# Kernel tuning notes

Measured on AMD Instinct MI355X. Metric: run time of the kernel, lower is better.

## Reference

```python
import jax, jax.numpy as jnp
import numpy as np

L, D, H, BS = 12, 768, 12, 512
VU, VD, NM, B = 512, 512, 438, 8
HD = D // H
EPS = 1e-5


def _ln(x, w, b):
    m = jnp.mean(x, axis=-1, keepdims=True)
    v = jnp.mean(jnp.square(x - m), axis=-1, keepdims=True)
    return (x - m) * jax.lax.rsqrt(v + EPS) * w + b


def setup_inputs() -> dict:
    key = jax.random.key(0)
    ks = jax.random.split(key, 16)
    s = 0.02
    inp = {
        'idx_up': jax.random.randint(ks[0], (B, BS), 0, VU),
        'idx_down': jax.random.randint(ks[1], (B, BS), 0, VD),
        'cond': jax.random.normal(ks[2], (B, BS, NM), dtype=jnp.float32),
        'tok_emb_up': s * jax.random.normal(ks[3], (VU, D), dtype=jnp.float32),
        'tok_emb_down': s * jax.random.normal(ks[4], (VD, D), dtype=jnp.float32),
        'pos_emb': s * jax.random.normal(ks[5], (1, 3 * BS, D), dtype=jnp.float32),
        'cond_w': s * jax.random.normal(ks[6], (NM, D), dtype=jnp.float32),
        'cond_b': jnp.zeros((D,), jnp.float32),
        'ln1_w': jnp.ones((L, D), jnp.float32),
        'ln1_b': jnp.zeros((L, D), jnp.float32),
        'ln2_w': jnp.ones((L, D), jnp.float32),
        'ln2_b': jnp.zeros((L, D), jnp.float32),
        'Wq': s * jax.random.normal(ks[7], (L, D, D), dtype=jnp.float32),
        'bq': jnp.zeros((L, D), jnp.float32),
        'Wk': s * jax.random.normal(ks[8], (L, D, D), dtype=jnp.float32),
        'bk': jnp.zeros((L, D), jnp.float32),
        'Wv': s * jax.random.normal(ks[9], (L, D, D), dtype=jnp.float32),
        'bv': jnp.zeros((L, D), jnp.float32),
        'Wp': s * jax.random.normal(ks[10], (L, D, D), dtype=jnp.float32),
        'bp': jnp.zeros((L, D), jnp.float32),
        'W1': s * jax.random.normal(ks[11], (L, D, 4 * D), dtype=jnp.float32),
        'b1': jnp.zeros((L, 4 * D), jnp.float32),
        'W2': s * jax.random.normal(ks[12], (L, 4 * D, D), dtype=jnp.float32),
        'b2': jnp.zeros((L, D), jnp.float32),
    }
    return inp


def reference(idx_up, idx_down, cond, tok_emb_up, tok_emb_down, pos_emb,
              cond_w, cond_b, ln1_w, ln1_b, ln2_w, ln2_b,
              Wq, bq, Wk, bk, Wv, bv, Wp, bp, W1, b1, W2, b2):
    b, t = idx_up.shape
    T = 3 * t
    # embeddings: [cond_emb | up | down] along seq
    x = jnp.concatenate([
        cond @ cond_w + cond_b,
        tok_emb_up[idx_up],
        tok_emb_down[idx_down],
    ], axis=1)
    pos = jnp.concatenate([
        pos_emb[:, :t, :],
        pos_emb[:, BS:BS + t, :],
        pos_emb[:, 2 * BS:2 * BS + t, :],
    ], axis=1)
    x = x + pos

    # 3x3-tiled causal mask over the three t-length segments
    tri = jnp.tril(jnp.ones((t, t), dtype=bool))
    mask = jnp.tile(tri, (3, 3))  # [T, T]
    scale = 1.0 / np.sqrt(HD)

    for l in range(L):
        h = _ln(x, ln1_w[l], ln1_b[l])
        q = (h @ Wq[l] + bq[l]).reshape(b, T, H, HD)
        k = (h @ Wk[l] + bk[l]).reshape(b, T, H, HD)
        v = (h @ Wv[l] + bv[l]).reshape(b, T, H, HD)
        att = jnp.einsum('bihd,bjhd->bhij', q, k) * scale
        att = jnp.where(mask, att, -jnp.inf)
        att = jax.nn.softmax(att, axis=-1)
        y = jnp.einsum('bhij,bjhd->bihd', att, v).reshape(b, T, D)
        x = x + (y @ Wp[l] + bp[l])

        h = _ln(x, ln2_w[l], ln2_b[l])
        h = jax.nn.gelu(h @ W1[l] + b1[l], approximate=False)
        x = x + (h @ W2[l] + b2[l])
    return x
```

## Files before the change

### kernel.cpp

```cpp
#include <hip/hip_runtime.h>
#include <cstdint>
#include <cstddef>

typedef uint16_t u16;
typedef __attribute__((ext_vector_type(8))) __bf16 bf16x8;
typedef __attribute__((ext_vector_type(4))) float f32x4;

#define DEVI static __device__ __forceinline__

DEVI u16 f2bf(float f) {
    union { float f; uint32_t u; } x; x.f = f;
    uint32_t r = (x.u + 0x7fffu + ((x.u >> 16) & 1u)) >> 16;
    return (u16)r;
}

DEVI void async_load16(const u16* g, const u16* l) {
    __builtin_amdgcn_global_load_lds(
        (__attribute__((address_space(1))) uint32_t*)(uintptr_t)g,
        (__attribute__((address_space(3))) uint32_t*)(uintptr_t)l,
        16, 0, 0);
}

enum { EP_QKV = 0, EP_RESID = 1, EP_GELU = 2, EP_COND = 3 };

template<int EP>
__global__ __launch_bounds__(256)
void gemm_k(const u16* __restrict__ A, const u16* __restrict__ Bt,
            int M, int N, int K,
            const float* __restrict__ bias0, const float* __restrict__ bias1,
            const float* __restrict__ bias2,
            float* __restrict__ xout, u16* __restrict__ bfout,
            const float* __restrict__ pos)
{
    __shared__ u16 As[128 * 32];
    __shared__ u16 Bs[128 * 32];
    const int tid = threadIdx.x;
    const int m0 = blockIdx.y * 128;
    const int n0 = blockIdx.x * 128;
    const int lane = tid & 63;
    const int wave = tid >> 6;
    const int quad = lane >> 4;
    const int l16 = lane & 15;
    const int wr = (wave >> 1) * 64;
    const int wc = (wave & 1) * 64;

    f32x4 acc[4][4] = {};

    const int srow = tid >> 2;
    const int sseg = tid & 3;
    const u16* aptr = A + (size_t)(m0 + srow) * K + sseg * 8;
    const u16* bptr = Bt + (size_t)(n0 + srow) * K + sseg * 8;

    for (int kb = 0; kb < K; kb += 32) {
        __syncthreads();
        async_load16(aptr + kb, As + tid * 8);
        async_load16(aptr + (size_t)64 * K + kb, As + 2048 + tid * 8);
        async_load16(bptr + kb, Bs + tid * 8);
        async_load16(bptr + (size_t)64 * K + kb, Bs + 2048 + tid * 8);
        __syncthreads();
        bf16x8 af[4], bfr[4];
        #pragma unroll
        for (int i = 0; i < 4; i++)
            af[i] = *(const bf16x8*)(As + (wr + i * 16 + l16) * 32 + quad * 8);
        #pragma unroll
        for (int i = 0; i < 4; i++)
            bfr[i] = *(const bf16x8*)(Bs + (wc + i * 16 + l16) * 32 + quad * 8);
        #pragma unroll
        for (int mi = 0; mi < 4; mi++)
            #pragma unroll
            for (int ni = 0; ni < 4; ni++)
                acc[mi][ni] = __builtin_amdgcn_mfma_f32_16x16x32_bf16(
                    af[mi], bfr[ni], acc[mi][ni], 0, 0, 0);
    }

    #pragma unroll
    for (int mi = 0; mi < 4; mi++) {
        const int rbase = m0 + wr + mi * 16 + quad * 4;
        #pragma unroll
        for (int ni = 0; ni < 4; ni++) {
            const int col = n0 + wc + ni * 16 + l16;
            float bias;
            if (EP == EP_QKV)
                bias = (col < 768) ? bias0[col]
                     : (col < 1536) ? bias1[col - 768] : bias2[col - 1536];
            else
                bias = bias0[col];
            #pragma unroll
            for (int r = 0; r < 4; r++) {
                const int row = rbase + r;
                float v = acc[mi][ni][r] + bias;
                if (EP == EP_QKV) {
                    bfout[(size_t)row * N + col] = f2bf(v);
                } else if (EP == EP_GELU) {
                    v = 0.5f * v * (1.0f + erff(v * 0.70710678f));
                    bfout[(size_t)row * N + col] = f2bf(v);
                } else if (EP == EP_RESID) {
                    xout[(size_t)row * N + col] += v;
                } else {
                    const int b = row >> 9, i = row & 511;
                    xout[((size_t)(b * 1536 + i)) * 768 + col] =
                        v + pos[(size_t)i * 768 + col];
                }
            }
        }
    }
}

__global__ __launch_bounds__(256)
void ln_k(const float* __restrict__ x, const float* __restrict__ w,
          const float* __restrict__ b, u16* __restrict__ h)
{
    const int row = blockIdx.x * 4 + (threadIdx.x >> 6);
    const int lane = threadIdx.x & 63;
    const float* xr = x + (size_t)row * 768;
    float vals[12];
    float s = 0.f;
    #pragma unroll
    for (int i = 0; i < 12; i++) { vals[i] = xr[lane + i * 64]; s += vals[i]; }
    #pragma unroll
    for (int o = 32; o; o >>= 1) s += __shfl_xor(s, o);
    const float mean = s * (1.f / 768.f);
    float vs = 0.f;
    #pragma unroll
    for (int i = 0; i < 12; i++) { float d = vals[i] - mean; vs += d * d; }
    #pragma unroll
    for (int o = 32; o; o >>= 1) vs += __shfl_xor(vs, o);
    const float rstd = rsqrtf(vs * (1.f / 768.f) + 1e-5f);
    u16* hr = h + (size_t)row * 768;
    #pragma unroll
    for (int i = 0; i < 12; i++) {
        const int c = lane + i * 64;
        hr[c] = f2bf((vals[i] - mean) * rstd * w[c] + b[c]);
    }
}

__global__ __launch_bounds__(256)
void attn_k(const u16* __restrict__ qkv, u16* __restrict__ y)
{
    __shared__ u16 Ks[64 * 64];
    __shared__ u16 Vt[64 * 64];
    __shared__ u16 Ps[4][16 * 72];
    const int qt = blockIdx.x, hh = blockIdx.y, b = blockIdx.z;
    const int tid = threadIdx.x, wave = tid >> 6, lane = tid & 63;
    const int quad = lane >> 4, l16 = lane & 15;
    const int l7 = l16 & 7;
    const size_t RS = 2304;
    const u16* qb  = qkv + (size_t)b * 1536 * RS + hh * 64;
    const u16* kbp = qb + 768;
    const u16* vbp = qb + 1536;

    bf16x8 qf[2];
    {
        const u16* qr = qb + (size_t)(qt * 64 + wave * 16 + l16) * RS + quad * 8;
        qf[0] = *(const bf16x8*)(qr);
        qf[1] = *(const bf16x8*)(qr + 32);
    }

    f32x4 o_acc[4] = {};
    float m_i = -1e30f, l_i = 0.f;
    const float scale = 0.125f;

    const int srow = tid >> 2;
    const int sseg = tid & 3;
    const int vkey = tid & 63, vw = tid >> 6;
    const int kmax = qt & 7;

    for (int seg3 = 0; seg3 < 3; seg3++) {
        for (int k8 = 0; k8 <= kmax; k8++) {
            const int kt = seg3 * 8 + k8;
            const bool diag = (k8 == kmax);
            __syncthreads();
            {
                const u16* krow = kbp + (size_t)(kt * 64 + srow) * RS;
                bf16x8 c0 = *(const bf16x8*)(krow + sseg * 8);
                bf16x8 c1 = *(const bf16x8*)(krow + (sseg + 4) * 8);
                const int sw = srow & 7;
                *(bf16x8*)(Ks + srow * 64 + ((sseg    ) ^ sw) * 8) = c0;
                *(bf16x8*)(Ks + srow * 64 + ((sseg + 4) ^ sw) * 8) = c1;
            }
            {
                const u16* vrow = vbp + (size_t)(kt * 64 + vkey) * RS;
                const int kc = vkey >> 3, ko = vkey & 7;
                #pragma unroll
                for (int i = 0; i < 2; i++) {
                    bf16x8 vv = *(const bf16x8*)(vrow + (vw + i * 4) * 8);
                    const u16* vr = (const u16*)&vv;
                    #pragma unroll
                    for (int j = 0; j < 8; j++) {
                        const int hd = (vw + i * 4) * 8 + j;
                        Vt[hd * 64 + ((kc ^ j) * 8) + ko] = vr[j];
                    }
                }
            }
            __syncthreads();

            f32x4 sacc[4] = {};
            #pragma unroll
            for (int st = 0; st < 2; st++)
                #pragma unroll
                for (int kb = 0; kb < 4; kb++) {
                    bf16x8 kf = *(const bf16x8*)(Ks + (kb * 16 + l16) * 64 +
                                    ((st * 4 + quad) ^ l7) * 8);
                    sacc[kb] = __builtin_amdgcn_mfma_f32_16x16x32_bf16(
                        kf, qf[st], sacc[kb], 0, 0, 0);
                }

            float sv[16];
            const int thr = wave * 16 + l16;
            #pragma unroll
            for (int kb = 0; kb < 4; kb++)
                #pragma unroll
                for (int r = 0; r < 4; r++) {
                    float v = sacc[kb][r] * scale;
                    if (diag && (kb * 16 + quad * 4 + r > thr)) v = -1e30f;
                    sv[kb * 4 + r] = v;
                }
            float mx = sv[0];
            #pragma unroll
            for (int i = 1; i < 16; i++) mx = fmaxf(mx, sv[i]);
            mx = fmaxf(mx, __shfl_xor(mx, 16));
            mx = fmaxf(mx, __shfl_xor(mx, 32));
            const float mnew = fmaxf(m_i, mx);
            const float alpha = __expf(m_i - mnew);
            float ps = 0.f;
            #pragma unroll
            for (int i = 0; i < 16; i++) { sv[i] = __expf(sv[i] - mnew); ps += sv[i]; }
            ps += __shfl_xor(ps, 16);
            ps += __shfl_xor(ps, 32);
            l_i = l_i * alpha + ps;
            m_i = mnew;
            #pragma unroll
            for (int n = 0; n < 4; n++) {
                o_acc[n][0] *= alpha; o_acc[n][1] *= alpha;
                o_acc[n][2] *= alpha; o_acc[n][3] *= alpha;
            }
            #pragma unroll
            for (int kb = 0; kb < 4; kb++) {
                ushort4 p4;
                p4.x = f2bf(sv[kb * 4 + 0]); p4.y = f2bf(sv[kb * 4 + 1]);
                p4.z = f2bf(sv[kb * 4 + 2]); p4.w = f2bf(sv[kb * 4 + 3]);
                *(ushort4*)(&Ps[wave][l16 * 72 + kb * 16 + quad * 4]) = p4;
            }
            #pragma unroll
            for (int st = 0; st < 2; st++) {
                bf16x8 pf = *(const bf16x8*)(&Ps[wave][l16 * 72 + st * 32 + quad * 8]);
                #pragma unroll
                for (int n = 0; n < 4; n++) {
                    bf16x8 vf = *(const bf16x8*)(Vt + (n * 16 + l16) * 64 +
                                    ((st * 4 + quad) ^ l7) * 8);
                    o_acc[n] = __builtin_amdgcn_mfma_f32_16x16x32_bf16(
                        vf, pf, o_acc[n], 0, 0, 0);
                }
            }
        }
    }

    const float inv = 1.f / l_i;
    u16* yr = y + ((size_t)b * 1536 + qt * 64 + wave * 16 + l16) * 768 + hh * 64;
    #pragma unroll
    for (int n = 0; n < 4; n++) {
        ushort4 o4;
        o4.x = f2bf(o_acc[n][0] * inv);
        o4.y = f2bf(o_acc[n][1] * inv);
        o4.z = f2bf(o_acc[n][2] * inv);
        o4.w = f2bf(o_acc[n][3] * inv);
        *(ushort4*)(yr + n * 16 + quad * 4) = o4;
    }
}

__global__ __launch_bounds__(256)
void cvt_layer_k(const float* __restrict__ Wq, const float* __restrict__ Wk,
                 const float* __restrict__ Wv, const float* __restrict__ Wp,
                 const float* __restrict__ W1, const float* __restrict__ W2,
                 u16* __restrict__ Wt)
{
    int id = blockIdx.x;
    const float* src; u16* dst; int Kd, Nd;
    if (id < 2304) {
        const int m = id / 576; id -= m * 576;
        src = (m == 0) ? Wq : (m == 1) ? Wk : (m == 2) ? Wv : Wp;
        dst = Wt + (size_t)m * 589824; Kd = 768; Nd = 768;
    } else if (id < 4608) {
        id -= 2304; src = W1; dst = Wt + (size_t)4 * 589824; Kd = 768; Nd = 3072;
    } else {
        id -= 4608; src = W2; dst = Wt + (size_t)4 * 589824 + 2359296; Kd = 3072; Nd = 768;
    }
    const int tn_n = Nd >> 5;
    const int tk = id / tn_n, tn = id - tk * tn_n;
    __shared__ float tile[32][33];
    const int tx = threadIdx.x & 31, ty = threadIdx.x >> 5;
    #pragma unroll
    for (int i = 0; i < 4; i++)
        tile[ty + i * 8][tx] = src[(size_t)(tk * 32 + ty + i * 8) * Nd + tn * 32 + tx];
    __syncthreads();
    #pragma unroll
    for (int i = 0; i < 4; i++)
        dst[(size_t)(tn * 32 + ty + i * 8) * Kd + tk * 32 + tx] = f2bf(tile[tx][ty + i * 8]);
}

__global__ void cvt_cond_k(const float* __restrict__ cond, u16* __restrict__ condb) {
    const int r = blockIdx.x, k = threadIdx.x;
    condb[(size_t)r * 448 + k] = (k < 438) ? f2bf(cond[(size_t)r * 438 + k]) : (u16)0;
}
__global__ void cvt_condw_k(const float* __restrict__ cw, u16* __restrict__ cwt) {
    const int n = blockIdx.x, k = threadIdx.x;
    cwt[(size_t)n * 448 + k] = (k < 438) ? f2bf(cw[(size_t)k * 768 + n]) : (u16)0;
}

__global__ void embed_k(const int* __restrict__ iu, const int* __restrict__ idn,
                        const float* __restrict__ eu, const float* __restrict__ ed,
                        const float* __restrict__ pos, float* __restrict__ x)
{
    const int t = blockIdx.x * 256 + threadIdx.x;
    const int d4 = t % 192;
    const int row = t / 192;
    const int b = row >> 10, pl = row & 1023;
    const float* src; int posrow;
    if (pl < 512) { src = eu + (size_t)iu[b * 512 + pl] * 768; posrow = 512 + pl; }
    else { src = ed + (size_t)idn[b * 512 + pl - 512] * 768; posrow = 1024 + (pl - 512); }
    float4 v = ((const float4*)src)[d4];
    const float4 p = ((const float4*)(pos + (size_t)posrow * 768))[d4];
    v.x += p.x; v.y += p.y; v.z += p.z; v.w += p.w;
    ((float4*)(x + ((size_t)b * 1536 + posrow) * 768))[d4] = v;
}

extern "C" void kernel_launch(void* const* d_in, const int* in_sizes, int n_in,
                              void* d_out, int out_size, void* d_ws, size_t ws_size,
                              hipStream_t stream)
{
    const int*   idx_up   = (const int*)d_in[0];
    const int*   idx_down = (const int*)d_in[1];
    const float* cond     = (const float*)d_in[2];
    const float* emb_up   = (const float*)d_in[3];
    const float* emb_down = (const float*)d_in[4];
    const float* pos      = (const float*)d_in[5];
    const float* cond_w   = (const float*)d_in[6];
    const float* cond_b   = (const float*)d_in[7];
    const float* ln1_w    = (const float*)d_in[8];
    const float* ln1_b    = (const float*)d_in[9];
    const float* ln2_w    = (const float*)d_in[10];
    const float* ln2_b    = (const float*)d_in[11];
    const float* Wq = (const float*)d_in[12]; const float* bq = (const float*)d_in[13];
    const float* Wk = (const float*)d_in[14]; const float* bk = (const float*)d_in[15];
    const float* Wv = (const float*)d_in[16]; const float* bv = (const float*)d_in[17];
    const float* Wp = (const float*)d_in[18]; const float* bp = (const float*)d_in[19];
    const float* W1 = (const float*)d_in[20]; const float* b1 = (const float*)d_in[21];
    const float* W2 = (const float*)d_in[22]; const float* b2 = (const float*)d_in[23];

    float* x = (float*)d_out;

    u16* h     = (u16*)d_ws;
    u16* qkv   = h + 9437184;
    u16* y     = qkv + 28311552;
    u16* h1    = y + 9437184;
    u16* Wt    = h1 + 37748736;
    u16* condb = Wt + 7077888;
    u16* cwt   = condb + 1835008;

    cvt_cond_k<<<4096, 448, 0, stream>>>(cond, condb);
    cvt_condw_k<<<768, 448, 0, stream>>>(cond_w, cwt);
    embed_k<<<6144, 256, 0, stream>>>(idx_up, idx_down, emb_up, emb_down, pos, x);
    gemm_k<EP_COND><<<dim3(6, 32), 256, 0, stream>>>(condb, cwt, 4096, 768, 448,
        cond_b, nullptr, nullptr, x, nullptr, pos);

    for (int l = 0; l < 12; l++) {
        cvt_layer_k<<<6912, 256, 0, stream>>>(
            Wq + (size_t)l * 589824, Wk + (size_t)l * 589824, Wv + (size_t)l * 589824,
            Wp + (size_t)l * 589824, W1 + (size_t)l * 2359296, W2 + (size_t)l * 2359296, Wt);
        ln_k<<<3072, 256, 0, stream>>>(x, ln1_w + l * 768, ln1_b + l * 768, h);
        gemm_k<EP_QKV><<<dim3(18, 96), 256, 0, stream>>>(h, Wt, 12288, 2304, 768,
            bq + l * 768, bk + l * 768, bv + l * 768, nullptr, qkv, nullptr);
        attn_k<<<dim3(24, 12, 8), 256, 0, stream>>>(qkv, y);
        gemm_k<EP_RESID><<<dim3(6, 96), 256, 0, stream>>>(y, Wt + (size_t)3 * 589824,
            12288, 768, 768, bp + l * 768, nullptr, nullptr, x, nullptr, nullptr);
        ln_k<<<3072, 256, 0, stream>>>(x, ln2_w + l * 768, ln2_b + l * 768, h);
        gemm_k<EP_GELU><<<dim3(24, 96), 256, 0, stream>>>(h, Wt + (size_t)4 * 589824,
            12288, 3072, 768, b1 + l * 3072, nullptr, nullptr, nullptr, h1, nullptr);
        gemm_k<EP_RESID><<<dim3(6, 96), 256, 0, stream>>>(h1,
            Wt + (size_t)4 * 589824 + 2359296, 12288, 768, 3072,
            b2 + l * 768, nullptr, nullptr, x, nullptr, nullptr);
    }
}
```

Measured before the change: 6.463 ms.

## Pair causal query tiles per block and read K fragments directly from global

Each attention block now handles two query tiles, a and 7-a, within a segment, so the causal work per block is equal and the grid is halved. The K tile is no longer staged in LDS; MFMA operands are loaded straight from global memory. The softmax scale and log2(e) are folded into Q so the kernel can use exp2f, and launch bounds request 4 blocks per CU. The trade-off is that each wave now reads K from global/L2 redundantly, and Q picks up an extra bf16 rounding after scaling.

```diff
diff --git a/kernel.cpp b/kernel.cpp
--- a/kernel.cpp
+++ b/kernel.cpp
@@ -134,137 +134,138 @@
     }
 }
 
-__global__ __launch_bounds__(256)
+__global__ __launch_bounds__(256, 4)
 void attn_k(const u16* __restrict__ qkv, u16* __restrict__ y)
 {
-    __shared__ u16 Ks[64 * 64];
     __shared__ u16 Vt[64 * 64];
     __shared__ u16 Ps[4][16 * 72];
-    const int qt = blockIdx.x, hh = blockIdx.y, b = blockIdx.z;
+    const int seg = blockIdx.x >> 2, a = blockIdx.x & 3;
+    const int hh = blockIdx.y, b = blockIdx.z;
     const int tid = threadIdx.x, wave = tid >> 6, lane = tid & 63;
-    const int quad = lane >> 4, l16 = lane & 15;
-    const int l7 = l16 & 7;
+    const int quad = lane >> 4, l16 = lane & 15, l7 = l16 & 7;
     const size_t RS = 2304;
     const u16* qb  = qkv + (size_t)b * 1536 * RS + hh * 64;
     const u16* kbp = qb + 768;
     const u16* vbp = qb + 1536;
-
-    bf16x8 qf[2];
-    {
-        const u16* qr = qb + (size_t)(qt * 64 + wave * 16 + l16) * RS + quad * 8;
-        qf[0] = *(const bf16x8*)(qr);
-        qf[1] = *(const bf16x8*)(qr + 32);
-    }
-
-    f32x4 o_acc[4] = {};
-    float m_i = -1e30f, l_i = 0.f;
-    const float scale = 0.125f;
-
-    const int srow = tid >> 2;
-    const int sseg = tid & 3;
     const int vkey = tid & 63, vw = tid >> 6;
-    const int kmax = qt & 7;
-
-    for (int seg3 = 0; seg3 < 3; seg3++) {
-        for (int k8 = 0; k8 <= kmax; k8++) {
-            const int kt = seg3 * 8 + k8;
-            const bool diag = (k8 == kmax);
-            __syncthreads();
-            {
-                const u16* krow = kbp + (size_t)(kt * 64 + srow) * RS;
-                bf16x8 c0 = *(const bf16x8*)(krow + sseg * 8);
-                bf16x8 c1 = *(const bf16x8*)(krow + (sseg + 4) * 8);
-                const int sw = srow & 7;
-                *(bf16x8*)(Ks + srow * 64 + ((sseg    ) ^ sw) * 8) = c0;
-                *(bf16x8*)(Ks + srow * 64 + ((sseg + 4) ^ sw) * 8) = c1;
-            }
-            {
-                const u16* vrow = vbp + (size_t)(kt * 64 + vkey) * RS;
-                const int kc = vkey >> 3, ko = vkey & 7;
-                #pragma unroll
-                for (int i = 0; i < 2; i++) {
-                    bf16x8 vv = *(const bf16x8*)(vrow + (vw + i * 4) * 8);
-                    const u16* vr = (const u16*)&vv;
-                    #pragma unroll
-                    for (int j = 0; j < 8; j++) {
-                        const int hd = (vw + i * 4) * 8 + j;
-                        Vt[hd * 64 + ((kc ^ j) * 8) + ko] = vr[j];
-                    }
-                }
-            }
-            __syncthreads();
-
-            f32x4 sacc[4] = {};
-            #pragma unroll
-            for (int st = 0; st < 2; st++)
-                #pragma unroll
-                for (int kb = 0; kb < 4; kb++) {
-                    bf16x8 kf = *(const bf16x8*)(Ks + (kb * 16 + l16) * 64 +
-                                    ((st * 4 + quad) ^ l7) * 8);
-                    sacc[kb] = __builtin_amdgcn_mfma_f32_16x16x32_bf16(
-                        kf, qf[st], sacc[kb], 0, 0, 0);
-                }
-
-            float sv[16];
-            const int thr = wave * 16 + l16;
-            #pragma unroll
-            for (int kb = 0; kb < 4; kb++)
-                #pragma unroll
-                for (int r = 0; r < 4; r++) {
-                    float v = sacc[kb][r] * scale;
-                    if (diag && (kb * 16 + quad * 4 + r > thr)) v = -1e30f;
-                    sv[kb * 4 + r] = v;
-                }
-            float mx = sv[0];
-            #pragma unroll
-            for (int i = 1; i < 16; i++) mx = fmaxf(mx, sv[i]);
-            mx = fmaxf(mx, __shfl_xor(mx, 16));
-            mx = fmaxf(mx, __shfl_xor(mx, 32));
-            const float mnew = fmaxf(m_i, mx);
-            const float alpha = __expf(m_i - mnew);
-            float ps = 0.f;
-            #pragma unroll
-            for (int i = 0; i < 16; i++) { sv[i] = __expf(sv[i] - mnew); ps += sv[i]; }
-            ps += __shfl_xor(ps, 16);
-            ps += __shfl_xor(ps, 32);
-            l_i = l_i * alpha + ps;
-            m_i = mnew;
-            #pragma unroll
-            for (int n = 0; n < 4; n++) {
-                o_acc[n][0] *= alpha; o_acc[n][1] *= alpha;
-                o_acc[n][2] *= alpha; o_acc[n][3] *= alpha;
-            }
-            #pragma unroll
-            for (int kb = 0; kb < 4; kb++) {
-                ushort4 p4;
-                p4.x = f2bf(sv[kb * 4 + 0]); p4.y = f2bf(sv[kb * 4 + 1]);
-                p4.z = f2bf(sv[kb * 4 + 2]); p4.w = f2bf(sv[kb * 4 + 3]);
-                *(ushort4*)(&Ps[wave][l16 * 72 + kb * 16 + quad * 4]) = p4;
-            }
+    const float SL2E = 0.125f * 1.44269504f;
+
+    for (int ph = 0; ph < 2; ph++) {
+        const int aa = ph ? 7 - a : a;
+        const int qt = seg * 8 + aa;
+
+        bf16x8 qf[2];
+        {
+            const u16* qr = qb + (size_t)(qt * 64 + wave * 16 + l16) * RS + quad * 8;
             #pragma unroll
             for (int st = 0; st < 2; st++) {
-                bf16x8 pf = *(const bf16x8*)(&Ps[wave][l16 * 72 + st * 32 + quad * 8]);
-                #pragma unroll
-                for (int n = 0; n < 4; n++) {
-                    bf16x8 vf = *(const bf16x8*)(Vt + (n * 16 + l16) * 64 +
-                                    ((st * 4 + quad) ^ l7) * 8);
-                    o_acc[n] = __builtin_amdgcn_mfma_f32_16x16x32_bf16(
-                        vf, pf, o_acc[n], 0, 0, 0);
-                }
+                bf16x8 qv = *(const bf16x8*)(qr + st * 32);
+                u16* qp = (u16*)&qv;
+                #pragma unroll
+                for (int j = 0; j < 8; j++) {
+                    union { float f; uint32_t u; } c; c.u = (uint32_t)qp[j] << 16;
+                    qp[j] = f2bf(c.f * SL2E);
+                }
+                qf[st] = qv;
             }
         }
-    }
-
-    const float inv = 1.f / l_i;
-    u16* yr = y + ((size_t)b * 1536 + qt * 64 + wave * 16 + l16) * 768 + hh * 64;
-    #pragma unroll
-    for (int n = 0; n < 4; n++) {
-        ushort4 o4;
-        o4.x = f2bf(o_acc[n][0] * inv);
-        o4.y = f2bf(o_acc[n][1] * inv);
-        o4.z = f2bf(o_acc[n][2] * inv);
-        o4.w = f2bf(o_acc[n][3] * inv);
-        *(ushort4*)(yr + n * 16 + quad * 4) = o4;
+
+        f32x4 o_acc[4] = {};
+        float m_i = -1e30f, l_i = 0.f;
+
+        for (int seg3 = 0; seg3 < 3; seg3++) {
+            for (int k8 = 0; k8 <= aa; k8++) {
+                const int kt = seg3 * 8 + k8;
+                const bool diag = (k8 == aa);
+                __syncthreads();
+                {
+                    const u16* vrow = vbp + (size_t)(kt * 64 + vkey) * RS;
+                    const int kc = vkey >> 3, ko = vkey & 7;
+                    #pragma unroll
+                    for (int i = 0; i < 2; i++) {
+                        bf16x8 vv = *(const bf16x8*)(vrow + (vw + i * 4) * 8);
+                        const u16* vr = (const u16*)&vv;
+                        #pragma unroll
+                        for (int j = 0; j < 8; j++) {
+                            const int hd = (vw + i * 4) * 8 + j;
+                            Vt[hd * 64 + ((kc ^ j) * 8) + ko] = vr[j];
+                        }
+                    }
+                }
+
+                f32x4 sacc[4] = {};
+                #pragma unroll
+                for (int st = 0; st < 2; st++)
+                    #pragma unroll
+                    for (int kb = 0; kb < 4; kb++) {
+                        bf16x8 kf = *(const bf16x8*)(kbp +
+                            (size_t)(kt * 64 + kb * 16 + l16) * RS + st * 32 + quad * 8);
+                        sacc[kb] = __builtin_amdgcn_mfma_f32_16x16x32_bf16(
+                            kf, qf[st], sacc[kb], 0, 0, 0);
+                    }
+
+                float sv[16];
+                const int thr = wave * 16 + l16;
+                #pragma unroll
+                for (int kb = 0; kb < 4; kb++)
+                    #pragma unroll
+                    for (int r = 0; r < 4; r++) {
+                        float v = sacc[kb][r];
+                        if (diag && (kb * 16 + quad * 4 + r > thr)) v = -1e30f;
+                        sv[kb * 4 + r] = v;
+                    }
+                float mx = sv[0];
+                #pragma unroll
+                for (int i = 1; i < 16; i++) mx = fmaxf(mx, sv[i]);
+                mx = fmaxf(mx, __shfl_xor(mx, 16));
+                mx = fmaxf(mx, __shfl_xor(mx, 32));
+                const float mnew = fmaxf(m_i, mx);
+                const float alpha = exp2f(m_i - mnew);
+                float ps = 0.f;
+                #pragma unroll
+                for (int i = 0; i < 16; i++) { sv[i] = exp2f(sv[i] - mnew); ps += sv[i]; }
+                ps += __shfl_xor(ps, 16);
+                ps += __shfl_xor(ps, 32);
+                l_i = l_i * alpha + ps;
+                m_i = mnew;
+                #pragma unroll
+                for (int n = 0; n < 4; n++) {
+                    o_acc[n][0] *= alpha; o_acc[n][1] *= alpha;
+                    o_acc[n][2] *= alpha; o_acc[n][3] *= alpha;
+                }
+                #pragma unroll
+                for (int kb = 0; kb < 4; kb++) {
+                    ushort4 p4;
+                    p4.x = f2bf(sv[kb * 4 + 0]); p4.y = f2bf(sv[kb * 4 + 1]);
+                    p4.z = f2bf(sv[kb * 4 + 2]); p4.w = f2bf(sv[kb * 4 + 3]);
+                    *(ushort4*)(&Ps[wave][l16 * 72 + kb * 16 + quad * 4]) = p4;
+                }
+                __syncthreads();
+                #pragma unroll
+                for (int st = 0; st < 2; st++) {
+                    bf16x8 pf = *(const bf16x8*)(&Ps[wave][l16 * 72 + st * 32 + quad * 8]);
+                    #pragma unroll
+                    for (int n = 0; n < 4; n++) {
+                        bf16x8 vf = *(const bf16x8*)(Vt + (n * 16 + l16) * 64 +
+                                        ((st * 4 + quad) ^ l7) * 8);
+                        o_acc[n] = __builtin_amdgcn_mfma_f32_16x16x32_bf16(
+                            vf, pf, o_acc[n], 0, 0, 0);
+                    }
+                }
+            }
+        }
+
+        const float inv = 1.f / l_i;
+        u16* yr = y + ((size_t)b * 1536 + qt * 64 + wave * 16 + l16) * 768 + hh * 64;
+        #pragma unroll
+        for (int n = 0; n < 4; n++) {
+            ushort4 o4;
+            o4.x = f2bf(o_acc[n][0] * inv);
+            o4.y = f2bf(o_acc[n][1] * inv);
+            o4.z = f2bf(o_acc[n][2] * inv);
+            o4.w = f2bf(o_acc[n][3] * inv);
+            *(ushort4*)(yr + n * 16 + quad * 4) = o4;
+        }
     }
 }
 
@@ -370,7 +371,7 @@
         ln_k<<<3072, 256, 0, stream>>>(x, ln1_w + l * 768, ln1_b + l * 768, h);
         gemm_k<EP_QKV><<<dim3(18, 96), 256, 0, stream>>>(h, Wt, 12288, 2304, 768,
             bq + l * 768, bk + l * 768, bv + l * 768, nullptr, qkv, nullptr);
-        attn_k<<<dim3(24, 12, 8), 256, 0, stream>>>(qkv, y);
+        attn_k<<<dim3(12, 12, 8), 256, 0, stream>>>(qkv, y);
         gemm_k<EP_RESID><<<dim3(6, 96), 256, 0, stream>>>(y, Wt + (size_t)3 * 589824,
             12288, 768, 768, bp + l * 768, nullptr, nullptr, x, nullptr, nullptr);
         ln_k<<<3072, 256, 0, stream>>>(x, ln2_w + l * 768, ln2_b + l * 768, h);
```

Measured after the change: 6.962 ms. 1.08x slower.
